# Kernel optimization log

Measured on AMD Instinct MI355X. Metric: run time of the kernel, lower is better.

Reference implementation:

```python
import jax, jax.numpy as jnp
import numpy as np

S, B, E = 2048, 2, 768
H = 12
D = E // H  # 64
SCALE = D ** -0.5


def setup_inputs() -> dict:
    key = jax.random.key(0)
    ks = jax.random.split(key, 10)
    inp = {
        "query": jax.random.normal(ks[0], (S, B, E), dtype=jnp.float32),
        "attn_bias": jax.random.normal(ks[1], (B * H, S, S), dtype=jnp.float32) * 0.1,
        "key_padding_mask": jax.random.randint(ks[2], (B, S), 0, 2).astype(bool),
        "Wq": jax.random.normal(ks[3], (E, E), dtype=jnp.float32) * (E ** -0.5),
        "bq": jnp.zeros((E,), dtype=jnp.float32),
        "Wk": jax.random.normal(ks[4], (E, E), dtype=jnp.float32) * (E ** -0.5),
        "bk": jnp.zeros((E,), dtype=jnp.float32),
        "Wv": jax.random.normal(ks[5], (E, E), dtype=jnp.float32) * (E ** -0.5),
        "bv": jnp.zeros((E,), dtype=jnp.float32),
        "Wo": jax.random.normal(ks[6], (E, E), dtype=jnp.float32) * (E ** -0.5),
        "bo": jnp.zeros((E,), dtype=jnp.float32),
    }
    return inp


def reference(query, attn_bias, key_padding_mask, Wq, bq, Wk, bk, Wv, bv, Wo, bo):
    s, b, e = query.shape
    # projections (torch Linear: x @ W.T + b)
    q = (query @ Wq.T + bq) * SCALE
    k = query @ Wk.T + bk
    v = query @ Wv.T + bv
    # [s, b, e] -> [b*h, s, d]
    def to_heads(x):
        return x.reshape(s, b * H, D).transpose(1, 0, 2)
    q, k, v = to_heads(q), to_heads(k), to_heads(v)
    # scores [b*h, s_q, s_k]
    scores = jnp.einsum('nqd,nkd->nqk', q, k) + attn_bias
    # key padding mask: [b, s_k] -> broadcast over heads and queries
    scores = scores.reshape(b, H, s, s)
    scores = jnp.where(key_padding_mask[:, None, None, :], -jnp.inf, scores)
    scores = scores.reshape(b * H, s, s)
    probs = jax.nn.softmax(scores, axis=-1)
    attn = jnp.einsum('nqk,nkd->nqd', probs, v)  # [b*h, s, d]
    attn = attn.transpose(1, 0, 2).reshape(s, b, e)
    return attn @ Wo.T + bo
```

## Files before the change

kernel.cpp:

```cpp
#include <hip/hip_runtime.h>
#include <hip/hip_bf16.h>

typedef __attribute__((ext_vector_type(8))) short s16x8;
typedef __attribute__((ext_vector_type(4))) float f32x4;
typedef unsigned short u16;
typedef unsigned int u32;

#define SDIM 2048
#define BDIM 2
#define HDIM 12
#define DDIM 64
#define EDIM 768
#define MDIM 4096
#define SCALE_Q 0.125f
#define KSPLIT 1024
#define NIT (KSPLIT / 32)
#define HFRAG 131072

static __device__ __forceinline__ f32x4 zero4() {
    f32x4 v; v[0] = v[1] = v[2] = v[3] = 0.f; return v;
}

static __device__ __forceinline__ u16 f2b(float x) {
    u32 u = __builtin_bit_cast(u32, x);
    u32 lsb = (u >> 16) & 1u;
    u += 0x7fffu + lsb;
    return (u16)(u >> 16);
}

static __device__ __forceinline__ f32x4 mfma16(s16x8 a, s16x8 b, f32x4 c) {
    return __builtin_amdgcn_mfma_f32_16x16x32_bf16(a, b, c, 0, 0, 0);
}

static __device__ __forceinline__ void gload_lds16(const void* g, void* l) {
    __builtin_amdgcn_global_load_lds(
        (const __attribute__((address_space(1))) void*)g,
        (__attribute__((address_space(3))) void*)l, 16, 0, 0);
}

__global__ void mask_bits_kernel(const u32* __restrict__ raw, u32* __restrict__ outbits) {
    __shared__ int okInt, okFloat;
    int t = threadIdx.x;
    if (t == 0) { okInt = 1; okFloat = 1; }
    __syncthreads();
    int li = 1, lf = 1;
    for (int i = t; i < 1024; i += blockDim.x) {
        u32 v = raw[i];
        if (v > 1u) li = 0;
        if (v != 0u && v != 0x3F800000u) lf = 0;
    }
    if (!li) atomicAnd(&okInt, 0);
    if (!lf) atomicAnd(&okFloat, 0);
    __syncthreads();
    const unsigned char* rb = (const unsigned char*)raw;
    if (t < (BDIM * SDIM) / 32) {
        u32 bits = 0;
        for (int j = 0; j < 32; ++j) {
            int i = t * 32 + j;
            int v;
            if (okInt)        v = (int)raw[i];
            else if (okFloat) v = (raw[i] != 0u) ? 1 : 0;
            else              v = (int)rb[i];
            bits |= (v ? 1u : 0u) << j;
        }
        outbits[t] = bits;
    }
}

__global__ __launch_bounds__(256) void conv_f32_bf16(
    const float* __restrict__ s, u16* __restrict__ d, int n8)
{
    int i = blockIdx.x * 256 + threadIdx.x;
    if (i >= n8) return;
    float4 x0 = ((const float4*)s)[(size_t)i * 2];
    float4 x1 = ((const float4*)s)[(size_t)i * 2 + 1];
    uint4 o;
    o.x = (u32)f2b(x0.x) | ((u32)f2b(x0.y) << 16);
    o.y = (u32)f2b(x0.z) | ((u32)f2b(x0.w) << 16);
    o.z = (u32)f2b(x1.x) | ((u32)f2b(x1.y) << 16);
    o.w = (u32)f2b(x1.z) | ((u32)f2b(x1.w) << 16);
    ((uint4*)d)[i] = o;
}

__global__ __launch_bounds__(256) void gemm_xwT(
    const u16* __restrict__ A, const u16* __restrict__ Wb,
    const float* __restrict__ bias, float scale,
    u16* __restrict__ out_sc, float* __restrict__ out_rm, int mode)
{
    __shared__ u16 Al[64 * 56];
    __shared__ u16 Bl[64 * 56];
    int tid = threadIdx.x;
    int mb = blockIdx.x * 64, nb = blockIdx.y * 64;
    int lane = tid & 63, w = tid >> 6;
    int r16 = lane & 15, g4 = lane >> 4;
    int wm = w >> 1, wn = w & 1;

    f32x4 acc[2][2];
    acc[0][0] = zero4(); acc[0][1] = zero4(); acc[1][0] = zero4(); acc[1][1] = zero4();

    int srow = tid >> 2, scol = (tid & 3) * 8;

    for (int kb = 0; kb < EDIM; kb += 32) {
        __syncthreads();
        *(uint4*)&Al[srow * 56 + scol] =
            *(const uint4*)&A[(size_t)(mb + srow) * EDIM + kb + scol];
        *(uint4*)&Bl[srow * 56 + scol] =
            *(const uint4*)&Wb[(size_t)(nb + srow) * EDIM + kb + scol];
        __syncthreads();
        s16x8 a[2], bb[2];
        #pragma unroll
        for (int mi = 0; mi < 2; ++mi)
            a[mi] = *(const s16x8*)&Al[(wm * 32 + mi * 16 + r16) * 56 + g4 * 8];
        #pragma unroll
        for (int ni = 0; ni < 2; ++ni)
            bb[ni] = *(const s16x8*)&Bl[(wn * 32 + ni * 16 + r16) * 56 + g4 * 8];
        #pragma unroll
        for (int mi = 0; mi < 2; ++mi)
            #pragma unroll
            for (int ni = 0; ni < 2; ++ni)
                acc[mi][ni] = mfma16(a[mi], bb[ni], acc[mi][ni]);
    }

    #pragma unroll
    for (int mi = 0; mi < 2; ++mi) {
        #pragma unroll
        for (int ni = 0; ni < 2; ++ni) {
            int n = nb + wn * 32 + ni * 16 + r16;
            float bv = bias[n];
            #pragma unroll
            for (int r = 0; r < 4; ++r) {
                int m = mb + wm * 32 + mi * 16 + g4 * 4 + r;
                float c = (acc[mi][ni][r] + bv) * scale;
                if (mode == 1) {
                    int s_ = m >> 1, b_ = m & 1, h_ = n >> 6, d_ = n & 63;
                    out_sc[((size_t)(b_ * HDIM + h_) * SDIM + s_) * DDIM + d_] = f2b(c);
                } else if (mode == 3) {
                    int s_ = m >> 1, b_ = m & 1, h_ = n >> 6, d_ = n & 63;
                    size_t p = (size_t)(b_ * HDIM + h_) * HFRAG
                             + (size_t)(s_ >> 4) * 1024 + (size_t)((d_ >> 5) & 1) * 512
                             + (size_t)(((d_ >> 3) & 3) * 16 + (s_ & 15)) * 8 + (d_ & 7);
                    out_sc[p] = f2b(c);
                } else if (mode == 4) {
                    int s_ = m >> 1, b_ = m & 1, h_ = n >> 6, d_ = n & 63;
                    size_t p = (size_t)(b_ * HDIM + h_) * HFRAG
                             + (size_t)(s_ >> 5) * 2048 + (size_t)((d_ >> 4) & 3) * 512
                             + (size_t)(((s_ >> 3) & 3) * 16 + (d_ & 15)) * 8 + (s_ & 7);
                    out_sc[p] = f2b(c);
                } else {
                    out_rm[(size_t)m * EDIM + n] = c;
                }
            }
        }
    }
}

struct KV { s16x8 k0, k1, k2, k3, v0, v1, v2, v3; };

__global__ __launch_bounds__(128) void attn_fused(
    const u16* __restrict__ qw, const u16* __restrict__ kf_g,
    const u16* __restrict__ vf_g, const float* __restrict__ bias,
    const u32* __restrict__ maskBits, u16* __restrict__ attn_out)
{
    __shared__ __align__(1024) unsigned char SM[21504];

    int flat = blockIdx.y * 64 + blockIdx.x;
    int virt = (flat & 7) * 192 + (flat >> 3);
    int qt = virt & 63, bh = virt >> 6;

    int tid = threadIdx.x;
    int w = tid >> 6, lane = tid & 63;
    int r16 = lane & 15, g4 = lane >> 4;
    int qbase = qt * 32;
    int b_ = bh / HDIM, h_ = bh % HDIM;
    const u16* Q  = qw   + (size_t)bh * SDIM * DDIM;
    const u16* KF = kf_g + (size_t)bh * HFRAG;
    const u16* VF = vf_g + (size_t)bh * HFRAG;
    const float* BrowQ = bias + (size_t)bh * SDIM * SDIM + (size_t)qbase * SDIM;
    const u32* mB = maskBits + b_ * (SDIM / 32);

    unsigned char* wb = SM + w * 10752;
    float* RingW = (float*)wb;
    u16*   Pl    = (u16*)(wb + 8192);

    s16x8 qf[2][2];
    #pragma unroll
    for (int h = 0; h < 2; ++h) {
        qf[h][0] = *(const s16x8*)&Q[(size_t)(qbase + 16 * h + r16) * DDIM + g4 * 8];
        qf[h][1] = *(const s16x8*)&Q[(size_t)(qbase + 16 * h + r16) * DDIM + g4 * 8 + 32];
    }

    f32x4 accO[2][4];
    #pragma unroll
    for (int h = 0; h < 2; ++h)
        #pragma unroll
        for (int dt = 0; dt < 4; ++dt) accO[h][dt] = zero4();
    float m_run[2] = {-1e30f, -1e30f}, l_run[2] = {0.f, 0.f};

    const int k0 = w * KSPLIT;

    auto issue_kv = [&](int t, KV& dst) {
        int tc = t < NIT ? t : NIT - 1;
        int kbn = k0 + tc * 32;
        const u16* KT = KF + (size_t)(kbn >> 4) * 1024;
        dst.k0 = *(const s16x8*)&KT[lane * 8];
        dst.k1 = *(const s16x8*)&KT[512 + lane * 8];
        dst.k2 = *(const s16x8*)&KT[1024 + lane * 8];
        dst.k3 = *(const s16x8*)&KT[1536 + lane * 8];
        const u16* VT = VF + (size_t)(kbn >> 5) * 2048;
        dst.v0 = *(const s16x8*)&VT[lane * 8];
        dst.v1 = *(const s16x8*)&VT[512 + lane * 8];
        dst.v2 = *(const s16x8*)&VT[1024 + lane * 8];
        dst.v3 = *(const s16x8*)&VT[1536 + lane * 8];
    };

    auto stage_bias = [&](int t) {
        int tc = t < NIT ? t : NIT - 1;
        int kb = k0 + tc * 32;
        unsigned char* slot = (unsigned char*)(RingW + (t & 1) * 1024);
        int sq = (lane & 7) ^ ((lane >> 3) & 7);
        #pragma unroll
        for (int j = 0; j < 4; ++j) {
            int row = j * 8 + (lane >> 3);
            gload_lds16(&BrowQ[(size_t)row * SDIM + kb + sq * 4], slot + j * 1024);
        }
    };

    auto compute = [&](int t, KV& cur) {
        u32 mw = mB[__builtin_amdgcn_readfirstlane((k0 + t * 32) >> 5)];
        const float* Bs = RingW + (t & 1) * 1024;
        f32x4 sc[2][2];
        #pragma unroll
        for (int h = 0; h < 2; ++h) {
            sc[h][0] = mfma16(cur.k1, qf[h][1], mfma16(cur.k0, qf[h][0], zero4()));
            sc[h][1] = mfma16(cur.k3, qf[h][1], mfma16(cur.k2, qf[h][0], zero4()));
        }
        #pragma unroll
        for (int h = 0; h < 2; ++h) {
            int rr = 16 * h + r16;
            #pragma unroll
            for (int kt = 0; kt < 2; ++kt) {
                float4 bc = *(const float4*)&Bs[rr * 32 + (((4 * kt + g4) ^ (r16 & 7)) * 4)];
                u32 mseg = (mw >> (16 * kt + 4 * g4)) & 0xF;
                sc[h][kt][0] = (mseg & 1) ? -1e30f : sc[h][kt][0] + bc.x;
                sc[h][kt][1] = (mseg & 2) ? -1e30f : sc[h][kt][1] + bc.y;
                sc[h][kt][2] = (mseg & 4) ? -1e30f : sc[h][kt][2] + bc.z;
                sc[h][kt][3] = (mseg & 8) ? -1e30f : sc[h][kt][3] + bc.w;
            }
        }
        #pragma unroll
        for (int h = 0; h < 2; ++h) {
            float pm = fmaxf(
                fmaxf(fmaxf(sc[h][0][0], sc[h][0][1]), fmaxf(sc[h][0][2], sc[h][0][3])),
                fmaxf(fmaxf(sc[h][1][0], sc[h][1][1]), fmaxf(sc[h][1][2], sc[h][1][3])));
            pm = fmaxf(pm, __shfl_xor(pm, 16));
            pm = fmaxf(pm, __shfl_xor(pm, 32));
            bool norescale = __all(pm <= m_run[h] + 4.f);
            float mn = norescale ? m_run[h] : fmaxf(m_run[h], pm);
            float p[8];
            #pragma unroll
            for (int kt = 0; kt < 2; ++kt)
                #pragma unroll
                for (int r = 0; r < 4; ++r)
                    p[kt * 4 + r] = __expf(sc[h][kt][r] - mn);
            float ps = ((p[0] + p[1]) + (p[2] + p[3])) + ((p[4] + p[5]) + (p[6] + p[7]));
            ps += __shfl_xor(ps, 16);
            ps += __shfl_xor(ps, 32);
            if (norescale) {
                l_run[h] += ps;
            } else {
                float alpha = __expf(m_run[h] - mn);
                l_run[h] = l_run[h] * alpha + ps;
                m_run[h] = mn;
                float aR0 = __shfl(alpha, g4 * 4 + 0);
                float aR1 = __shfl(alpha, g4 * 4 + 1);
                float aR2 = __shfl(alpha, g4 * 4 + 2);
                float aR3 = __shfl(alpha, g4 * 4 + 3);
                #pragma unroll
                for (int dt = 0; dt < 4; ++dt) {
                    accO[h][dt][0] *= aR0;
                    accO[h][dt][1] *= aR1;
                    accO[h][dt][2] *= aR2;
                    accO[h][dt][3] *= aR3;
                }
            }
            int rr = 16 * h + r16;
            #pragma unroll
            for (int kt = 0; kt < 2; ++kt) {
                uint2 pv;
                pv.x = (u32)f2b(p[kt * 4 + 0]) | ((u32)f2b(p[kt * 4 + 1]) << 16);
                pv.y = (u32)f2b(p[kt * 4 + 2]) | ((u32)f2b(p[kt * 4 + 3]) << 16);
                *(uint2*)&Pl[rr * 40 + kt * 16 + g4 * 4] = pv;
            }
        }
        #pragma unroll
        for (int h = 0; h < 2; ++h) {
            s16x8 pf = *(const s16x8*)&Pl[(16 * h + r16) * 40 + g4 * 8];
            accO[h][0] = mfma16(pf, cur.v0, accO[h][0]);
            accO[h][1] = mfma16(pf, cur.v1, accO[h][1]);
            accO[h][2] = mfma16(pf, cur.v2, accO[h][2]);
            accO[h][3] = mfma16(pf, cur.v3, accO[h][3]);
        }
    };

    KV A, B;
    issue_kv(0, A);
    stage_bias(0);

    for (int t = 0; t < NIT; t += 2) {
        issue_kv(t + 1, B);
        stage_bias(t + 1);
        asm volatile("s_waitcnt vmcnt(12)" ::: "memory");
        __builtin_amdgcn_sched_barrier(0);
        compute(t, A);

        issue_kv(t + 2, A);
        stage_bias(t + 2);
        asm volatile("s_waitcnt vmcnt(12)" ::: "memory");
        __builtin_amdgcn_sched_barrier(0);
        compute(t + 1, B);
    }

    __syncthreads();
    float* As = (float*)SM;
    float* Ml = (float*)(SM + 17408);
    float* Ll = Ml + 64;
    #pragma unroll
    for (int h = 0; h < 2; ++h)
        #pragma unroll
        for (int dt = 0; dt < 4; ++dt)
            #pragma unroll
            for (int r = 0; r < 4; ++r)
                As[(size_t)(w * 32 + 16 * h + g4 * 4 + r) * 68 + dt * 16 + r16] = accO[h][dt][r];
    if (g4 == 0) {
        #pragma unroll
        for (int h = 0; h < 2; ++h) {
            Ml[w * 32 + 16 * h + r16] = m_run[h];
            Ll[w * 32 + 16 * h + r16] = l_run[h];
        }
    }
    __syncthreads();

    #pragma unroll
    for (int h = 0; h < 2; ++h) {
        #pragma unroll
        for (int dg = 0; dg < 2; ++dg) {
            int d = w * 32 + dg * 16 + r16;
            #pragma unroll
            for (int r = 0; r < 4; ++r) {
                int q = 16 * h + g4 * 4 + r;
                float m0 = Ml[q], m1 = Ml[32 + q];
                float mt = fmaxf(m0, m1);
                float e0 = __expf(m0 - mt), e1 = __expf(m1 - mt);
                float lt = Ll[q] * e0 + Ll[32 + q] * e1;
                float o = (As[(size_t)q * 68 + d] * e0 + As[(size_t)(32 + q) * 68 + d] * e1) / lt;
                attn_out[((size_t)(qbase + q) * BDIM + b_) * EDIM + h_ * DDIM + d] = f2b(o);
            }
        }
    }
}

extern "C" void kernel_launch(void* const* d_in, const int* in_sizes, int n_in,
                              void* d_out, int out_size, void* d_ws, size_t ws_size,
                              hipStream_t stream) {
    const float* query     = (const float*)d_in[0];
    const float* attn_bias = (const float*)d_in[1];
    const u32*   mask_raw  = (const u32*)d_in[2];
    const float* Wq = (const float*)d_in[3];
    const float* bq = (const float*)d_in[4];
    const float* Wk = (const float*)d_in[5];
    const float* bk = (const float*)d_in[6];
    const float* Wv = (const float*)d_in[7];
    const float* bv = (const float*)d_in[8];
    const float* Wo = (const float*)d_in[9];
    const float* bo = (const float*)d_in[10];
    float* out = (float*)d_out;

    char* ws = (char*)d_ws;
    u32* maskB = (u32*)ws;
    const size_t HEADSZ = (size_t)BDIM * HDIM * SDIM * DDIM;
    const size_t WSZ = (size_t)EDIM * EDIM;
    u16* qws = (u16*)(ws + 16384);
    u16* kws = qws + HEADSZ;
    u16* vws = kws + HEADSZ;
    u16* aws = vws + HEADSZ;
    u16* qbf = aws;
    u16* wWq = aws + HEADSZ;
    u16* wWk = wWq + WSZ;
    u16* wWv = wWk + WSZ;
    u16* wWo = wWv + WSZ;

    mask_bits_kernel<<<1, 256, 0, stream>>>(mask_raw, maskB);

    conv_f32_bf16<<<(int)(MDIM * EDIM / 8 / 256), 256, 0, stream>>>(query, qbf, MDIM * EDIM / 8);
    conv_f32_bf16<<<(int)(WSZ / 8 / 256), 256, 0, stream>>>(Wq, wWq, (int)(WSZ / 8));
    conv_f32_bf16<<<(int)(WSZ / 8 / 256), 256, 0, stream>>>(Wk, wWk, (int)(WSZ / 8));
    conv_f32_bf16<<<(int)(WSZ / 8 / 256), 256, 0, stream>>>(Wv, wWv, (int)(WSZ / 8));
    conv_f32_bf16<<<(int)(WSZ / 8 / 256), 256, 0, stream>>>(Wo, wWo, (int)(WSZ / 8));

    dim3 gg(MDIM / 64, EDIM / 64);
    gemm_xwT<<<gg, 256, 0, stream>>>(qbf, wWq, bq, SCALE_Q, qws, nullptr, 1);
    gemm_xwT<<<gg, 256, 0, stream>>>(qbf, wWk, bk, 1.0f,    kws, nullptr, 3);
    gemm_xwT<<<gg, 256, 0, stream>>>(qbf, wWv, bv, 1.0f,    vws, nullptr, 4);

    dim3 ga(64, BDIM * HDIM);
    attn_fused<<<ga, 128, 0, stream>>>(qws, kws, vws, attn_bias, maskB, aws);

    gemm_xwT<<<gg, 256, 0, stream>>>(aws, wWo, bo, 1.0f, nullptr, out, 0);
}
```

Baseline: 233.3 us.

## Fuse QKV projections into one launch, use direct-to-LDS loads, add MFMA priority

Merges the three Q/K/V projection GEMMs into a single kernel launch whose grid spans all three weight matrices, and gives the output projection its own specialised kernel. Both GEMMs now stage tiles with global-to-LDS loads in a fragment-major layout and step K by 64 instead of 32. The attention kernel also raises wave priority around its MFMA blocks. Together these aim to cut launch overhead and LDS staging cost, at the price of an unpipelined vmcnt(0) wait on every K step.

```diff
diff --git a/kernel.cpp b/kernel.cpp
--- a/kernel.cpp
+++ b/kernel.cpp
@@ -82,43 +82,54 @@
     ((uint4*)d)[i] = o;
 }
 
-__global__ __launch_bounds__(256) void gemm_xwT(
-    const u16* __restrict__ A, const u16* __restrict__ Wb,
-    const float* __restrict__ bias, float scale,
-    u16* __restrict__ out_sc, float* __restrict__ out_rm, int mode)
+__global__ __launch_bounds__(256) void gemm_qkv(
+    const u16* __restrict__ A,
+    const u16* __restrict__ wq, const u16* __restrict__ wk, const u16* __restrict__ wv,
+    const float* __restrict__ bq, const float* __restrict__ bk, const float* __restrict__ bv,
+    u16* __restrict__ qout, u16* __restrict__ kout, u16* __restrict__ vout)
 {
-    __shared__ u16 Al[64 * 56];
-    __shared__ u16 Bl[64 * 56];
+    __shared__ u16 Al[4096];
+    __shared__ u16 Bl[4096];
     int tid = threadIdx.x;
-    int mb = blockIdx.x * 64, nb = blockIdx.y * 64;
     int lane = tid & 63, w = tid >> 6;
     int r16 = lane & 15, g4 = lane >> 4;
     int wm = w >> 1, wn = w & 1;
+    int mb = blockIdx.x * 64;
+    int nbg = blockIdx.y * 64;
+    int mid = nbg / EDIM;
+    int nb = nbg - mid * EDIM;
+    const u16* W = (mid == 0) ? wq : (mid == 1) ? wk : wv;
+    const float* bias = (mid == 0) ? bq : (mid == 1) ? bk : bv;
+    float scale = (mid == 0) ? SCALE_Q : 1.0f;
 
     f32x4 acc[2][2];
     acc[0][0] = zero4(); acc[0][1] = zero4(); acc[1][0] = zero4(); acc[1][1] = zero4();
 
-    int srow = tid >> 2, scol = (tid & 3) * 8;
-
-    for (int kb = 0; kb < EDIM; kb += 32) {
+    for (int kb = 0; kb < EDIM; kb += 64) {
         __syncthreads();
-        *(uint4*)&Al[srow * 56 + scol] =
-            *(const uint4*)&A[(size_t)(mb + srow) * EDIM + kb + scol];
-        *(uint4*)&Bl[srow * 56 + scol] =
-            *(const uint4*)&Wb[(size_t)(nb + srow) * EDIM + kb + scol];
+        #pragma unroll
+        for (int j = 0; j < 2; ++j) {
+            int c = w * 2 + j;
+            gload_lds16(&A[(size_t)(mb + lane) * EDIM + kb + c * 8], (char*)Al + c * 1024);
+            gload_lds16(&W[(size_t)(nb + lane) * EDIM + kb + c * 8], (char*)Bl + c * 1024);
+        }
+        asm volatile("s_waitcnt vmcnt(0)" ::: "memory");
         __syncthreads();
-        s16x8 a[2], bb[2];
-        #pragma unroll
-        for (int mi = 0; mi < 2; ++mi)
-            a[mi] = *(const s16x8*)&Al[(wm * 32 + mi * 16 + r16) * 56 + g4 * 8];
-        #pragma unroll
-        for (int ni = 0; ni < 2; ++ni)
-            bb[ni] = *(const s16x8*)&Bl[(wn * 32 + ni * 16 + r16) * 56 + g4 * 8];
-        #pragma unroll
-        for (int mi = 0; mi < 2; ++mi)
+        #pragma unroll
+        for (int kk = 0; kk < 2; ++kk) {
+            s16x8 a[2], b[2];
+            #pragma unroll
+            for (int mi = 0; mi < 2; ++mi)
+                a[mi] = *(const s16x8*)&Al[(kk * 4 + g4) * 512 + (wm * 32 + mi * 16 + r16) * 8];
             #pragma unroll
             for (int ni = 0; ni < 2; ++ni)
-                acc[mi][ni] = mfma16(a[mi], bb[ni], acc[mi][ni]);
+                b[ni] = *(const s16x8*)&Bl[(kk * 4 + g4) * 512 + (wn * 32 + ni * 16 + r16) * 8];
+            #pragma unroll
+            for (int mi = 0; mi < 2; ++mi)
+                #pragma unroll
+                for (int ni = 0; ni < 2; ++ni)
+                    acc[mi][ni] = mfma16(a[mi], b[ni], acc[mi][ni]);
+        }
     }
 
     #pragma unroll
@@ -126,29 +137,82 @@
         #pragma unroll
         for (int ni = 0; ni < 2; ++ni) {
             int n = nb + wn * 32 + ni * 16 + r16;
-            float bv = bias[n];
+            float bv_ = bias[n];
             #pragma unroll
             for (int r = 0; r < 4; ++r) {
                 int m = mb + wm * 32 + mi * 16 + g4 * 4 + r;
-                float c = (acc[mi][ni][r] + bv) * scale;
-                if (mode == 1) {
-                    int s_ = m >> 1, b_ = m & 1, h_ = n >> 6, d_ = n & 63;
-                    out_sc[((size_t)(b_ * HDIM + h_) * SDIM + s_) * DDIM + d_] = f2b(c);
-                } else if (mode == 3) {
-                    int s_ = m >> 1, b_ = m & 1, h_ = n >> 6, d_ = n & 63;
+                float c = (acc[mi][ni][r] + bv_) * scale;
+                int s_ = m >> 1, b_ = m & 1, h_ = n >> 6, d_ = n & 63;
+                if (mid == 0) {
+                    qout[((size_t)(b_ * HDIM + h_) * SDIM + s_) * DDIM + d_] = f2b(c);
+                } else if (mid == 1) {
                     size_t p = (size_t)(b_ * HDIM + h_) * HFRAG
                              + (size_t)(s_ >> 4) * 1024 + (size_t)((d_ >> 5) & 1) * 512
                              + (size_t)(((d_ >> 3) & 3) * 16 + (s_ & 15)) * 8 + (d_ & 7);
-                    out_sc[p] = f2b(c);
-                } else if (mode == 4) {
-                    int s_ = m >> 1, b_ = m & 1, h_ = n >> 6, d_ = n & 63;
+                    kout[p] = f2b(c);
+                } else {
                     size_t p = (size_t)(b_ * HDIM + h_) * HFRAG
                              + (size_t)(s_ >> 5) * 2048 + (size_t)((d_ >> 4) & 3) * 512
                              + (size_t)(((s_ >> 3) & 3) * 16 + (d_ & 15)) * 8 + (s_ & 7);
-                    out_sc[p] = f2b(c);
-                } else {
-                    out_rm[(size_t)m * EDIM + n] = c;
+                    vout[p] = f2b(c);
                 }
+            }
+        }
+    }
+}
+
+__global__ __launch_bounds__(256) void gemm_out(
+    const u16* __restrict__ A, const u16* __restrict__ Wb,
+    const float* __restrict__ bias, float* __restrict__ out_rm)
+{
+    __shared__ u16 Al[4096];
+    __shared__ u16 Bl[4096];
+    int tid = threadIdx.x;
+    int lane = tid & 63, w = tid >> 6;
+    int r16 = lane & 15, g4 = lane >> 4;
+    int wm = w >> 1, wn = w & 1;
+    int mb = blockIdx.x * 64, nb = blockIdx.y * 64;
+
+    f32x4 acc[2][2];
+    acc[0][0] = zero4(); acc[0][1] = zero4(); acc[1][0] = zero4(); acc[1][1] = zero4();
+
+    for (int kb = 0; kb < EDIM; kb += 64) {
+        __syncthreads();
+        #pragma unroll
+        for (int j = 0; j < 2; ++j) {
+            int c = w * 2 + j;
+            gload_lds16(&A[(size_t)(mb + lane) * EDIM + kb + c * 8], (char*)Al + c * 1024);
+            gload_lds16(&Wb[(size_t)(nb + lane) * EDIM + kb + c * 8], (char*)Bl + c * 1024);
+        }
+        asm volatile("s_waitcnt vmcnt(0)" ::: "memory");
+        __syncthreads();
+        #pragma unroll
+        for (int kk = 0; kk < 2; ++kk) {
+            s16x8 a[2], b[2];
+            #pragma unroll
+            for (int mi = 0; mi < 2; ++mi)
+                a[mi] = *(const s16x8*)&Al[(kk * 4 + g4) * 512 + (wm * 32 + mi * 16 + r16) * 8];
+            #pragma unroll
+            for (int ni = 0; ni < 2; ++ni)
+                b[ni] = *(const s16x8*)&Bl[(kk * 4 + g4) * 512 + (wn * 32 + ni * 16 + r16) * 8];
+            #pragma unroll
+            for (int mi = 0; mi < 2; ++mi)
+                #pragma unroll
+                for (int ni = 0; ni < 2; ++ni)
+                    acc[mi][ni] = mfma16(a[mi], b[ni], acc[mi][ni]);
+        }
+    }
+
+    #pragma unroll
+    for (int mi = 0; mi < 2; ++mi) {
+        #pragma unroll
+        for (int ni = 0; ni < 2; ++ni) {
+            int n = nb + wn * 32 + ni * 16 + r16;
+            float bv_ = bias[n];
+            #pragma unroll
+            for (int r = 0; r < 4; ++r) {
+                int m = mb + wm * 32 + mi * 16 + g4 * 4 + r;
+                out_rm[(size_t)m * EDIM + n] = acc[mi][ni][r] + bv_;
             }
         }
     }
@@ -229,11 +293,13 @@
         u32 mw = mB[__builtin_amdgcn_readfirstlane((k0 + t * 32) >> 5)];
         const float* Bs = RingW + (t & 1) * 1024;
         f32x4 sc[2][2];
+        __builtin_amdgcn_s_setprio(1);
         #pragma unroll
         for (int h = 0; h < 2; ++h) {
             sc[h][0] = mfma16(cur.k1, qf[h][1], mfma16(cur.k0, qf[h][0], zero4()));
             sc[h][1] = mfma16(cur.k3, qf[h][1], mfma16(cur.k2, qf[h][0], zero4()));
         }
+        __builtin_amdgcn_s_setprio(0);
         #pragma unroll
         for (int h = 0; h < 2; ++h) {
             int rr = 16 * h + r16;
@@ -292,6 +358,7 @@
                 *(uint2*)&Pl[rr * 40 + kt * 16 + g4 * 4] = pv;
             }
         }
+        __builtin_amdgcn_s_setprio(1);
         #pragma unroll
         for (int h = 0; h < 2; ++h) {
             s16x8 pf = *(const s16x8*)&Pl[(16 * h + r16) * 40 + g4 * 8];
@@ -300,6 +367,7 @@
             accO[h][2] = mfma16(pf, cur.v2, accO[h][2]);
             accO[h][3] = mfma16(pf, cur.v3, accO[h][3]);
         }
+        __builtin_amdgcn_s_setprio(0);
     };
 
     KV A, B;
@@ -397,13 +465,12 @@
     conv_f32_bf16<<<(int)(WSZ / 8 / 256), 256, 0, stream>>>(Wv, wWv, (int)(WSZ / 8));
     conv_f32_bf16<<<(int)(WSZ / 8 / 256), 256, 0, stream>>>(Wo, wWo, (int)(WSZ / 8));
 
-    dim3 gg(MDIM / 64, EDIM / 64);
-    gemm_xwT<<<gg, 256, 0, stream>>>(qbf, wWq, bq, SCALE_Q, qws, nullptr, 1);
-    gemm_xwT<<<gg, 256, 0, stream>>>(qbf, wWk, bk, 1.0f,    kws, nullptr, 3);
-    gemm_xwT<<<gg, 256, 0, stream>>>(qbf, wWv, bv, 1.0f,    vws, nullptr, 4);
+    dim3 gq(MDIM / 64, (3 * EDIM) / 64);
+    gemm_qkv<<<gq, 256, 0, stream>>>(qbf, wWq, wWk, wWv, bq, bk, bv, qws, kws, vws);
 
     dim3 ga(64, BDIM * HDIM);
     attn_fused<<<ga, 128, 0, stream>>>(qws, kws, vws, attn_bias, maskB, aws);
 
-    gemm_xwT<<<gg, 256, 0, stream>>>(aws, wWo, bo, 1.0f, nullptr, out, 0);
-}
+    dim3 go(MDIM / 64, EDIM / 64);
+    gemm_out<<<go, 256, 0, stream>>>(aws, wWo, bo, out);
+}
```

New measurement: 247.4 us. 1.06x slower.
